# Kernel tuning notes

Measured on AMD Instinct MI355X. Metric: run time of the kernel, lower is better.

## Reference

```python
import jax, jax.numpy as jnp
import numpy as np

NEG_SLOPE = 0.2  # PyG GATConv default negative_slope
EPS = 1e-16      # PyG softmax denominator eps


def gat_layer(x, src, dst, W, b, a_src, a_dst, n_nodes):
    # x: [N, Fin]; W: [Fout, Fin]; a_src/a_dst: [Fout] (heads=1, concat)
    h = x @ W.T                                   # [N, Fout]
    al_s = h @ a_src                              # [N]
    al_d = h @ a_dst                              # [N]
    e = jax.nn.leaky_relu(al_s[src] + al_d[dst], NEG_SLOPE)   # [E]
    m = jax.lax.stop_gradient(
        jax.ops.segment_max(e, dst, num_segments=n_nodes))   # stable softmax per target
    ex = jnp.exp(e - m[dst])
    denom = jax.ops.segment_sum(ex, dst, num_segments=n_nodes)
    alpha = ex / (denom[dst] + EPS)               # [E]
    out = jax.ops.segment_sum(alpha[:, None] * h[src], dst, num_segments=n_nodes)
    return out + b


def reference(x, edge_index, W0, b0, asrc0, adst0, W1, b1, asrc1, adst1):
    B, N, _ = x.shape
    # GATConv adds self-loops by default
    loops = jnp.arange(N, dtype=edge_index.dtype)
    src = jnp.concatenate([edge_index[0], loops])
    dst = jnp.concatenate([edge_index[1], loops])

    def per_graph(xb):
        h = jax.nn.relu(gat_layer(xb, src, dst, W0, b0, asrc0, adst0, N))
        h = jax.nn.relu(gat_layer(h, src, dst, W1, b1, asrc1, adst1, N))
        return h

    return jax.vmap(per_graph)(x)  # [B, N, Fout]


def setup_inputs() -> dict:
    key = jax.random.key(0)
    ks = jax.random.split(key, 10)
    B, N, E = 4, 10000, 320000
    F0, F1, F2 = 256, 256, 128
    x = jax.random.normal(ks[0], (B, N, F0), dtype=jnp.float32)
    edge_index = jax.random.randint(ks[1], (2, E), 0, N, dtype=jnp.int64)
    s0 = 1.0 / np.sqrt(F0)
    s1 = 1.0 / np.sqrt(F1)
    return {
        "x": x,
        "edge_index": edge_index,
        "W0": jax.random.normal(ks[2], (F1, F0), dtype=jnp.float32) * s0,
        "b0": jnp.zeros((F1,), dtype=jnp.float32),
        "asrc0": jax.random.normal(ks[3], (F1,), dtype=jnp.float32) * s1,
        "adst0": jax.random.normal(ks[4], (F1,), dtype=jnp.float32) * s1,
        "W1": jax.random.normal(ks[5], (F2, F1), dtype=jnp.float32) * s1,
        "b1": jnp.zeros((F2,), dtype=jnp.float32),
        "asrc1": jax.random.normal(ks[6], (F2,), dtype=jnp.float32) / np.sqrt(F2),
        "adst1": jax.random.normal(ks[7], (F2,), dtype=jnp.float32) / np.sqrt(F2),
    }
```

## Files before the change

kernel.cpp:

```cpp
#include <hip/hip_runtime.h>
#include <hip/hip_bf16.h>

#define NN 10000
#define EE 320000
#define BB 4
#define F0 256
#define F1 256
#define F2 128
#define ETOT (EE + NN)

typedef __attribute__((ext_vector_type(8))) short bf16x8;
typedef __attribute__((ext_vector_type(4))) float f32x4;
typedef unsigned short us8 __attribute__((ext_vector_type(8)));

__device__ inline unsigned short f2bf_rn(float f) {
    unsigned int u = __float_as_uint(f);
    unsigned int r = (u + 0x7fffu + ((u >> 16) & 1u)) >> 16;
    return (unsigned short)r;
}
__device__ inline float bf2f(unsigned short s) {
    return __uint_as_float(((unsigned int)s) << 16);
}

__global__ void count_kernel(const int* __restrict__ ei, int* __restrict__ deg) {
    int id = blockIdx.x * blockDim.x + threadIdx.x;
    if (id >= ETOT) return;
    int dst = (id < EE) ? ei[EE + id] : (id - EE);
    atomicAdd(&deg[dst], 1);
}

__global__ void scan_kernel(const int* __restrict__ deg, int* __restrict__ rowstart) {
    __shared__ int part[256];
    int t = threadIdx.x;
    const int CH = (NN + 255) / 256;
    int lo = t * CH, hi = min(lo + CH, NN);
    int s = 0;
    for (int i = lo; i < hi; i++) s += deg[i];
    part[t] = s;
    __syncthreads();
    for (int off = 1; off < 256; off <<= 1) {
        int v = (t >= off) ? part[t - off] : 0;
        __syncthreads();
        part[t] += v;
        __syncthreads();
    }
    int run = (t == 0) ? 0 : part[t - 1];
    for (int i = lo; i < hi; i++) { int d = deg[i]; rowstart[i] = run; run += d; }
    if (t == 255) rowstart[NN] = run;
}

__global__ void scatter_kernel(const int* __restrict__ ei,
                               const int* __restrict__ rowstart,
                               int* __restrict__ fill,
                               int* __restrict__ sorted_src) {
    int id = blockIdx.x * blockDim.x + threadIdx.x;
    if (id >= ETOT) return;
    int src, dst;
    if (id < EE) { src = ei[id]; dst = ei[EE + id]; }
    else         { src = dst = id - EE; }
    int pos = rowstart[dst] + atomicAdd(&fill[dst], 1);
    sorted_src[pos] = src;
}

__global__ __launch_bounds__(256) void conv_split_w(const float* __restrict__ W0,
                                                    const float* __restrict__ W1,
                                                    unsigned short* __restrict__ W02,
                                                    unsigned short* __restrict__ W12) {
    int id = blockIdx.x * 256 + threadIdx.x;
    if (id >= (F1 + F2) * 64) return;
    int r = id >> 6, c4 = (id & 63) << 2;
    const float* src;
    unsigned short* dst;
    if (r < F1) { src = W0 + (size_t)r * 256;        dst = W02 + (size_t)r * 512; }
    else        { src = W1 + (size_t)(r - F1) * 256; dst = W12 + (size_t)(r - F1) * 512; }
    float4 v = *(const float4*)(src + c4);
    ushort4 hi, lo;
    hi.x = f2bf_rn(v.x); lo.x = f2bf_rn(v.x - bf2f(hi.x));
    hi.y = f2bf_rn(v.y); lo.y = f2bf_rn(v.y - bf2f(hi.y));
    hi.z = f2bf_rn(v.z); lo.z = f2bf_rn(v.z - bf2f(hi.z));
    hi.w = f2bf_rn(v.w); lo.w = f2bf_rn(v.w - bf2f(hi.w));
    *(ushort4*)(dst + c4) = hi;
    *(ushort4*)(dst + 256 + c4) = lo;
}

template <int NT, int XF32>
__global__ __launch_bounds__(256) void gemm_db(
    const float* __restrict__ Af,
    const unsigned short* __restrict__ A2,
    const unsigned short* __restrict__ B2,
    unsigned short* __restrict__ C,
    const float* __restrict__ asrc,
    const float* __restrict__ adst,
    float* __restrict__ als2,
    float* __restrict__ ald2) {
    __shared__ unsigned short sbuf[15360];
    unsigned short* Ah = sbuf;
    unsigned short* Al = sbuf + 2560;
    unsigned short* Bh = sbuf + 5120;
    unsigned short* Bl = sbuf + 10240;

    int tid = threadIdx.x;
    int wave = tid >> 6, lane = tid & 63;
    int wm = wave & 1, wn = wave >> 1;
    int lq = lane >> 4, lm = lane & 15;
    int bm = blockIdx.x * 64;
    int by = blockIdx.y;
    int bn = by * 128;

    f32x4 acc[2][4];
#pragma unroll
    for (int i = 0; i < 2; i++)
#pragma unroll
        for (int j = 0; j < 4; j++) {
            acc[i][j][0] = 0.f; acc[i][j][1] = 0.f;
            acc[i][j][2] = 0.f; acc[i][j][3] = 0.f;
        }

    int r0 = tid >> 2, sub = tid & 3;
    const unsigned short* aSrc2 = A2 + (size_t)(bm + r0) * 512 + sub * 8;
    const float* aSrcF = Af + (size_t)(bm + r0) * 256 + sub * 8;
    const unsigned short* bSrc0 = B2 + (size_t)(bn + r0) * 512 + sub * 8;
    const unsigned short* bSrc1 = B2 + (size_t)(bn + r0 + 64) * 512 + sub * 8;
    int lda = r0 * 40 + sub * 8;
    int ldb0 = r0 * 40 + sub * 8;
    int ldb1 = (r0 + 64) * 40 + sub * 8;

    uint4 pAh, pAl, pBh0, pBh1, pBl0, pBl1;
    float4 pF0, pF1;

    auto loadreg = [&](int c) {
        int o = c * 32;
        if (XF32) {
            pF0 = *(const float4*)(aSrcF + o);
            pF1 = *(const float4*)(aSrcF + o + 4);
        } else {
            pAh = *(const uint4*)(aSrc2 + o);
            pAl = *(const uint4*)(aSrc2 + 256 + o);
        }
        pBh0 = *(const uint4*)(bSrc0 + o);       pBh1 = *(const uint4*)(bSrc1 + o);
        pBl0 = *(const uint4*)(bSrc0 + 256 + o); pBl1 = *(const uint4*)(bSrc1 + 256 + o);
    };
    auto writereg = [&]() {
        if (XF32) {
            float fa[8];
            *(float4*)&fa[0] = pF0; *(float4*)&fa[4] = pF1;
            us8 hs, ls;
#pragma unroll
            for (int u = 0; u < 8; u++) {
                unsigned short hv = f2bf_rn(fa[u]);
                hs[u] = hv;
                ls[u] = f2bf_rn(fa[u] - bf2f(hv));
            }
            *(us8*)(Ah + lda) = hs;
            *(us8*)(Al + lda) = ls;
        } else {
            *(uint4*)(Ah + lda) = pAh;
            *(uint4*)(Al + lda) = pAl;
        }
        *(uint4*)(Bh + ldb0) = pBh0; *(uint4*)(Bh + ldb1) = pBh1;
        *(uint4*)(Bl + ldb0) = pBl0; *(uint4*)(Bl + ldb1) = pBl1;
    };

    loadreg(0);
#pragma unroll 1
    for (int c = 0; c < 8; c++) {
        __syncthreads();
        writereg();
        __syncthreads();
        if (c < 7) loadreg(c + 1);

        bf16x8 afh[2], afl[2];
#pragma unroll
        for (int i = 0; i < 2; i++) {
            int row = wm * 32 + i * 16 + lm;
            afh[i] = *(const bf16x8*)(Ah + row * 40 + lq * 8);
            afl[i] = *(const bf16x8*)(Al + row * 40 + lq * 8);
        }
#pragma unroll
        for (int j = 0; j < 4; j++) {
            int row = wn * 64 + j * 16 + lm;
            bf16x8 bh = *(const bf16x8*)(Bh + row * 40 + lq * 8);
            bf16x8 bl = *(const bf16x8*)(Bl + row * 40 + lq * 8);
#pragma unroll
            for (int i = 0; i < 2; i++) {
                acc[i][j] = __builtin_amdgcn_mfma_f32_16x16x32_bf16(afh[i], bh, acc[i][j], 0, 0, 0);
                acc[i][j] = __builtin_amdgcn_mfma_f32_16x16x32_bf16(afl[i], bh, acc[i][j], 0, 0, 0);
                acc[i][j] = __builtin_amdgcn_mfma_f32_16x16x32_bf16(afh[i], bl, acc[i][j], 0, 0, 0);
            }
        }
    }

    __syncthreads();

    unsigned short* Cs = sbuf;
#pragma unroll
    for (int i = 0; i < 2; i++) {
#pragma unroll
        for (int rr = 0; rr < 4; rr++) {
            int row = wm * 32 + i * 16 + lq * 4 + rr;
#pragma unroll
            for (int j = 0; j < 4; j++)
                Cs[row * 136 + wn * 64 + j * 16 + lm] = f2bf_rn(acc[i][j][rr]);
        }
    }
    __syncthreads();

    {
        int r = tid >> 2;
        int cseg = (tid & 3) * 32;
        float s = 0.f, d = 0.f;
#pragma unroll
        for (int c8 = 0; c8 < 4; c8++) {
            bf16x8 v8 = *(const bf16x8*)(Cs + r * 136 + cseg + c8 * 8);
#pragma unroll
            for (int u = 0; u < 8; u++) {
                float v = bf2f((unsigned short)v8[u]);
                s += v * asrc[bn + cseg + c8 * 8 + u];
                d += v * adst[bn + cseg + c8 * 8 + u];
            }
        }
        s += __shfl_xor(s, 1); d += __shfl_xor(d, 1);
        s += __shfl_xor(s, 2); d += __shfl_xor(d, 2);
        if ((tid & 3) == 0) {
            als2[(size_t)(bm + r) * 2 + by] = s;
            ald2[(size_t)(bm + r) * 2 + by] = d;
        }
        if (NT == 128 && (tid & 3) == 1) {
            als2[(size_t)(bm + r) * 2 + 1] = 0.f;
            ald2[(size_t)(bm + r) * 2 + 1] = 0.f;
        }
    }

#pragma unroll
    for (int k = 0; k < 4; k++) {
        int u = k * 256 + tid;
        int row = u >> 4, q = u & 15;
        *(uint4*)(C + (size_t)(bm + row) * NT + bn + q * 8) = *(const uint4*)(Cs + row * 136 + q * 8);
    }
}

template <int F, int OUTMODE>
__global__ __launch_bounds__(256) void agg_kernel(const unsigned short* __restrict__ h,
                                                  const float* __restrict__ als2,
                                                  const float* __restrict__ ald2,
                                                  const int* __restrict__ rowstart,
                                                  const int* __restrict__ sorted_src,
                                                  const float* __restrict__ bias,
                                                  float* __restrict__ out,
                                                  unsigned short* __restrict__ out2) {
    constexpr int V = F / 64;
    typedef unsigned short usv __attribute__((ext_vector_type(V)));
    typedef float fvec __attribute__((ext_vector_type(V)));

    int wid = (blockIdx.x * blockDim.x + threadIdx.x) >> 6;
    int lane = threadIdx.x & 63;
    int b = wid / NN;
    int n = wid - b * NN;

    const float2* als_b = (const float2*)als2 + (size_t)b * NN;
    float2 d2 = ((const float2*)ald2)[wid];
    float aldn = d2.x + d2.y;
    int rs = rowstart[n];
    int deg = rowstart[n + 1] - rs;
    const unsigned short* hb = h + (size_t)b * NN * F;

    fvec acc;
#pragma unroll
    for (int u = 0; u < V; u++) acc[u] = 0.f;
    float sum = 0.f;

    for (int c0 = 0; c0 < deg; c0 += 64) {
        int j = c0 + lane;
        float ex = 0.f;
        int srcj = 0;
        if (j < deg) {
            srcj = sorted_src[rs + j];
            float2 a2 = als_b[srcj];
            float e = a2.x + a2.y + aldn;
            e = e > 0.f ? e : 0.2f * e;
            ex = __expf(e);
        }
        sum += ex;
        int cnt = min(64, deg - c0);

        int nfull = cnt >> 4;
        for (int g = 0; g < nfull; g++) {
            int bse = g << 4;
            int s[16]; float w[16];
#pragma unroll
            for (int i = 0; i < 16; i++) {
                s[i] = __shfl(srcj, bse + i);
                w[i] = __shfl(ex, bse + i);
            }
            usv r[16];
#pragma unroll
            for (int i = 0; i < 16; i++)
                r[i] = *(const usv*)(hb + (size_t)s[i] * F + lane * V);
#pragma unroll
            for (int i = 0; i < 16; i++)
#pragma unroll
                for (int u = 0; u < V; u++) acc[u] += w[i] * bf2f(r[i][u]);
        }
        for (int bse = nfull << 4; bse < cnt; bse += 4) {
            int s[4]; float w[4];
#pragma unroll
            for (int i = 0; i < 4; i++) {
                s[i] = __shfl(srcj, bse + i);
                w[i] = __shfl(ex, bse + i);
            }
            usv r[4];
#pragma unroll
            for (int i = 0; i < 4; i++)
                r[i] = *(const usv*)(hb + (size_t)s[i] * F + lane * V);
#pragma unroll
            for (int i = 0; i < 4; i++)
#pragma unroll
                for (int u = 0; u < V; u++) acc[u] += w[i] * bf2f(r[i][u]);
        }
    }
#pragma unroll
    for (int off = 32; off; off >>= 1) sum += __shfl_xor(sum, off);
    float inv = 1.0f / (sum + 1e-16f);

    fvec r;
#pragma unroll
    for (int u = 0; u < V; u++) {
        float v = acc[u] * inv + bias[lane * V + u];
        r[u] = fmaxf(v, 0.f);
    }
    if (OUTMODE == 0) {
        *(fvec*)(out + (size_t)wid * F + lane * V) = r;
    } else {
        ushort4 hi, lo;
        hi.x = f2bf_rn(r[0]); lo.x = f2bf_rn(r[0] - bf2f(hi.x));
        hi.y = f2bf_rn(r[1]); lo.y = f2bf_rn(r[1] - bf2f(hi.y));
        hi.z = f2bf_rn(r[2]); lo.z = f2bf_rn(r[2] - bf2f(hi.z));
        hi.w = f2bf_rn(r[3]); lo.w = f2bf_rn(r[3] - bf2f(hi.w));
        unsigned short* o = out2 + (size_t)wid * 2 * F;
        *(ushort4*)(o + lane * 4) = hi;
        *(ushort4*)(o + F + lane * 4) = lo;
    }
}

extern "C" void kernel_launch(void* const* d_in, const int* in_sizes, int n_in,
                              void* d_out, int out_size, void* d_ws, size_t ws_size,
                              hipStream_t stream) {
    const float* x     = (const float*)d_in[0];
    const int*   ei    = (const int*)d_in[1];
    const float* W0    = (const float*)d_in[2];
    const float* b0    = (const float*)d_in[3];
    const float* asrc0 = (const float*)d_in[4];
    const float* adst0 = (const float*)d_in[5];
    const float* W1    = (const float*)d_in[6];
    const float* b1    = (const float*)d_in[7];
    const float* asrc1 = (const float*)d_in[8];
    const float* adst1 = (const float*)d_in[9];
    float* outp = (float*)d_out;

    const int M = BB * NN;

    size_t off = 0;
    char* base = (char*)d_ws;
    auto alloc = [&](size_t bytes) {
        void* p = base + off;
        off += (bytes + 255) & ~(size_t)255;
        return p;
    };
    int*   deg        = (int*)alloc((size_t)NN * 4);
    int*   fill       = (int*)alloc((size_t)NN * 4);
    int*   rowstart   = (int*)alloc((size_t)(NN + 1) * 4);
    int*   sorted_src = (int*)alloc((size_t)ETOT * 4);
    unsigned short* A2  = (unsigned short*)alloc((size_t)M * 512 * 2);
    unsigned short* W02 = (unsigned short*)alloc((size_t)F1 * 512 * 2);
    unsigned short* W12 = (unsigned short*)alloc((size_t)F2 * 512 * 2);
    unsigned short* h   = (unsigned short*)alloc((size_t)M * F1 * 2);
    float* als2       = (float*)alloc((size_t)M * 2 * 4);
    float* ald2       = (float*)alloc((size_t)M * 2 * 4);

    hipMemsetAsync(deg, 0, (char*)fill - (char*)deg + (size_t)NN * 4, stream);

    int egrid = (ETOT + 255) / 256;
    count_kernel<<<egrid, 256, 0, stream>>>(ei, deg);
    scan_kernel<<<1, 256, 0, stream>>>(deg, rowstart);
    scatter_kernel<<<egrid, 256, 0, stream>>>(ei, rowstart, fill, sorted_src);

    conv_split_w<<<((F1 + F2) * 64 + 255) / 256, 256, 0, stream>>>(W0, W1, W02, W12);

    int wgrid = (M * 64) / 256;

    gemm_db<F1, 1><<<dim3(625, F1 / 128), 256, 0, stream>>>(x, nullptr, W02, h,
                                                            asrc0, adst0, als2, ald2);
    agg_kernel<F1, 1><<<wgrid, 256, 0, stream>>>(h, als2, ald2, rowstart, sorted_src, b0,
                                                 nullptr, A2 );

    gemm_db<F2, 0><<<dim3(625, F2 / 128), 256, 0, stream>>>(nullptr, A2, W12, h,
                                                            asrc1, adst1, als2, ald2);
    agg_kernel<F2, 0><<<wgrid, 256, 0, stream>>>(h, als2, ald2, rowstart, sorted_src, b1,
                                                 outp, nullptr);
}
```

Baseline: 311.0 us.

## Split wavefront into lane groups gathering 16-byte rows of several edges

The aggregation kernel now has each lane load 8 bf16 features (16 bytes) instead of F/64 features. The wavefront is split into F/8-lane groups that each handle a different neighbour edge at the same time. Partial sums are combined with xor-shuffles at the end, and only group 0 writes the output. The aim is wider, fewer gather loads per edge and more edges in flight. The cost is an extra cross-lane reduction, and short tails do wasted weight-zero loads from row 0.

```diff
diff --git a/kernel.cpp b/kernel.cpp
--- a/kernel.cpp
+++ b/kernel.cpp
@@ -248,14 +248,15 @@
                                                   const float* __restrict__ bias,
                                                   float* __restrict__ out,
                                                   unsigned short* __restrict__ out2) {
-    constexpr int V = F / 64;
-    typedef unsigned short usv __attribute__((ext_vector_type(V)));
-    typedef float fvec __attribute__((ext_vector_type(V)));
+    constexpr int LPE = F / 8;
+    constexpr int G = 64 / LPE;
 
     int wid = (blockIdx.x * blockDim.x + threadIdx.x) >> 6;
     int lane = threadIdx.x & 63;
     int b = wid / NN;
     int n = wid - b * NN;
+    int g = lane / LPE;
+    int fb = lane % LPE;
 
     const float2* als_b = (const float2*)als2 + (size_t)b * NN;
     float2 d2 = ((const float2*)ald2)[wid];
@@ -264,9 +265,9 @@
     int deg = rowstart[n + 1] - rs;
     const unsigned short* hb = h + (size_t)b * NN * F;
 
-    fvec acc;
-#pragma unroll
-    for (int u = 0; u < V; u++) acc[u] = 0.f;
+    float acc[8];
+#pragma unroll
+    for (int u = 0; u < 8; u++) acc[u] = 0.f;
     float sum = 0.f;
 
     for (int c0 = 0; c0 < deg; c0 += 64) {
@@ -283,62 +284,57 @@
         sum += ex;
         int cnt = min(64, deg - c0);
 
-        int nfull = cnt >> 4;
-        for (int g = 0; g < nfull; g++) {
-            int bse = g << 4;
-            int s[16]; float w[16];
-#pragma unroll
-            for (int i = 0; i < 16; i++) {
-                s[i] = __shfl(srcj, bse + i);
-                w[i] = __shfl(ex, bse + i);
-            }
-            usv r[16];
-#pragma unroll
-            for (int i = 0; i < 16; i++)
-                r[i] = *(const usv*)(hb + (size_t)s[i] * F + lane * V);
-#pragma unroll
-            for (int i = 0; i < 16; i++)
-#pragma unroll
-                for (int u = 0; u < V; u++) acc[u] += w[i] * bf2f(r[i][u]);
-        }
-        for (int bse = nfull << 4; bse < cnt; bse += 4) {
-            int s[4]; float w[4];
-#pragma unroll
-            for (int i = 0; i < 4; i++) {
-                s[i] = __shfl(srcj, bse + i);
-                w[i] = __shfl(ex, bse + i);
-            }
-            usv r[4];
-#pragma unroll
-            for (int i = 0; i < 4; i++)
-                r[i] = *(const usv*)(hb + (size_t)s[i] * F + lane * V);
-#pragma unroll
-            for (int i = 0; i < 4; i++)
-#pragma unroll
-                for (int u = 0; u < V; u++) acc[u] += w[i] * bf2f(r[i][u]);
+        for (int bse = 0; bse < cnt; bse += 8 * G) {
+            int s[8];
+#pragma unroll
+            for (int i = 0; i < 8; i++)
+                s[i] = __shfl(srcj, bse + i * G + g);
+            us8 r[8];
+#pragma unroll
+            for (int i = 0; i < 8; i++)
+                r[i] = *(const us8*)(hb + (size_t)s[i] * F + fb * 8);
+#pragma unroll
+            for (int i = 0; i < 8; i++) {
+                float w = __shfl(ex, bse + i * G + g);
+#pragma unroll
+                for (int u = 0; u < 8; u++)
+                    acc[u] += w * bf2f((unsigned short)r[i][u]);
+            }
         }
     }
 #pragma unroll
     for (int off = 32; off; off >>= 1) sum += __shfl_xor(sum, off);
+#pragma unroll
+    for (int m = LPE; m < 64; m <<= 1)
+#pragma unroll
+        for (int u = 0; u < 8; u++) acc[u] += __shfl_xor(acc[u], m);
+
     float inv = 1.0f / (sum + 1e-16f);
 
-    fvec r;
-#pragma unroll
-    for (int u = 0; u < V; u++) {
-        float v = acc[u] * inv + bias[lane * V + u];
-        r[u] = fmaxf(v, 0.f);
-    }
-    if (OUTMODE == 0) {
-        *(fvec*)(out + (size_t)wid * F + lane * V) = r;
-    } else {
-        ushort4 hi, lo;
-        hi.x = f2bf_rn(r[0]); lo.x = f2bf_rn(r[0] - bf2f(hi.x));
-        hi.y = f2bf_rn(r[1]); lo.y = f2bf_rn(r[1] - bf2f(hi.y));
-        hi.z = f2bf_rn(r[2]); lo.z = f2bf_rn(r[2] - bf2f(hi.z));
-        hi.w = f2bf_rn(r[3]); lo.w = f2bf_rn(r[3] - bf2f(hi.w));
-        unsigned short* o = out2 + (size_t)wid * 2 * F;
-        *(ushort4*)(o + lane * 4) = hi;
-        *(ushort4*)(o + F + lane * 4) = lo;
+    float rv[8];
+#pragma unroll
+    for (int u = 0; u < 8; u++) {
+        float v = acc[u] * inv + bias[fb * 8 + u];
+        rv[u] = fmaxf(v, 0.f);
+    }
+
+    if (g == 0) {
+        if (OUTMODE == 0) {
+            float* o = out + (size_t)wid * F + fb * 8;
+            *(float4*)(o) = make_float4(rv[0], rv[1], rv[2], rv[3]);
+            *(float4*)(o + 4) = make_float4(rv[4], rv[5], rv[6], rv[7]);
+        } else {
+            us8 hi8, lo8;
+#pragma unroll
+            for (int u = 0; u < 8; u++) {
+                unsigned short hv = f2bf_rn(rv[u]);
+                hi8[u] = hv;
+                lo8[u] = f2bf_rn(rv[u] - bf2f(hv));
+            }
+            unsigned short* o = out2 + (size_t)wid * 2 * F + fb * 8;
+            *(us8*)(o) = hi8;
+            *(us8*)(o + F) = lo8;
+        }
     }
 }
 
```

Measured after the change: 304.7 us. 1.02x faster.
